# Kernel tuning notes

Measured on AMD Instinct MI355X. Metric: run time of the kernel, lower is better.

## Reference

```python
import jax, jax.numpy as jnp
import numpy as np

V = 8000; TZ = 128; TU = 256; B = 64; H = 1024; E = 512; DG = 64
GI = E + 2 * H + DG  # GRU input size = embed + z_ctx + u_ctx + degree


def _build_sparse_z(rng):
    # faithful vectorized version of get_sparse_selective_input (minus vocab SLOT branch)
    z_np = rng.integers(0, V + 10, size=(TZ, B))  # some ids >= V -> OOV copy path
    res = np.full((TZ, B, V + TZ), 1e-10, np.float32)
    w = z_np[:-1]                                   # [TZ-1, B]
    cond = (w == 2) | (w >= V)
    ti, bi = np.meshgrid(np.arange(TZ - 1), np.arange(B), indexing='ij')
    col = np.where(cond, V + ti, w)
    val = np.where(cond, np.float32(5.0), np.float32(1.0))
    res[ti + 1, bi, col] = val
    return jnp.asarray(res.transpose(1, 0, 2))      # [B, TZ, V+TZ]


def setup_inputs():
    key = jax.random.key(0)
    ks = jax.random.split(key, 16)
    s = 0.02
    iv = 1.0 / np.sqrt(H)
    return dict(
        z_enc_out=jax.random.normal(ks[0], (TZ, B, H), jnp.float32),
        u_enc_out=jax.random.normal(ks[1], (TU, B, H), jnp.float32),
        m_t_input=jax.random.randint(ks[2], (1, B), 0, V),
        degree_input=jax.random.normal(ks[3], (B, DG), jnp.float32),
        last_hidden=jax.random.normal(ks[4], (1, B, H), jnp.float32),
        sparse_z_input=_build_sparse_z(np.random.default_rng(0)),
        emb_W=jax.random.normal(ks[5], (V, E), jnp.float32) * s,
        attn_z_W=jax.random.normal(ks[6], (H, 2 * H), jnp.float32) * s,
        attn_z_b=jnp.zeros((H,), jnp.float32),
        attn_z_v=jax.random.normal(ks[7], (H,), jnp.float32) * iv,
        attn_u_W=jax.random.normal(ks[8], (H, 2 * H), jnp.float32) * s,
        attn_u_b=jnp.zeros((H,), jnp.float32),
        attn_u_v=jax.random.normal(ks[9], (H,), jnp.float32) * iv,
        gru_Wih=jax.random.normal(ks[10], (3 * H, GI), jnp.float32) * s,
        gru_Whh=jax.random.normal(ks[11], (3 * H, H), jnp.float32) * s,
        gru_bih=jnp.zeros((3 * H,), jnp.float32),
        gru_bhh=jnp.zeros((3 * H,), jnp.float32),
        proj_W=jax.random.normal(ks[12], (V, 3 * H), jnp.float32) * s,
        proj_b=jnp.zeros((V,), jnp.float32),
        copy2_W=jax.random.normal(ks[13], (H, H), jnp.float32) * s,
        copy2_b=jnp.zeros((H,), jnp.float32),
    )


def _attn(hidden, enc, W, b, v):
    # hidden [1,B,H], enc [T,B,H] -> context [1,B,H] (Bahdanau additive attention)
    enc_b = jnp.transpose(enc, (1, 0, 2))                       # [B,T,H]
    Hrep = jnp.broadcast_to(jnp.transpose(hidden, (1, 0, 2)), enc_b.shape)
    energy = jnp.tanh(jnp.concatenate([Hrep, enc_b], -1) @ W.T + b)  # [B,T,H]
    scores = jnp.einsum('bth,h->bt', energy, v)[:, None, :]    # [B,1,T]
    alpha = jax.nn.softmax(scores, axis=2)
    ctx = jnp.einsum('bit,bth->bih', alpha, enc_b)              # [B,1,H]
    return jnp.transpose(ctx, (1, 0, 2))                        # [1,B,H]


def _gru_step(x, h, Wih, Whh, bih, bhh):
    # single step, torch gate order (r, z, n)
    gi = x @ Wih.T + bih
    gh = h @ Whh.T + bhh
    ir, iz, inn = jnp.split(gi, 3, -1)
    hr, hz, hn = jnp.split(gh, 3, -1)
    r = jax.nn.sigmoid(ir + hr)
    z = jax.nn.sigmoid(iz + hz)
    n = jnp.tanh(inn + r * hn)
    return (1.0 - z) * n + z * h


def reference(z_enc_out, u_enc_out, m_t_input, degree_input, last_hidden,
              sparse_z_input, emb_W, attn_z_W, attn_z_b, attn_z_v,
              attn_u_W, attn_u_b, attn_u_v, gru_Wih, gru_Whh, gru_bih, gru_bhh,
              proj_W, proj_b, copy2_W, copy2_b):
    m_embed = emb_W[m_t_input]                                  # [1,B,E]
    z_ctx = _attn(last_hidden, z_enc_out, attn_z_W, attn_z_b, attn_z_v)  # [1,B,H]
    u_ctx = _attn(last_hidden, u_enc_out, attn_u_W, attn_u_b, attn_u_v)  # [1,B,H]
    gru_in = jnp.concatenate([m_embed, u_ctx, z_ctx, degree_input[None]], axis=2)
    gru_out = _gru_step(gru_in, last_hidden, gru_Wih, gru_Whh, gru_bih, gru_bhh)
    new_hidden = gru_out                                        # single-layer GRU, 1 step
    gen_score = (jnp.concatenate([z_ctx, u_ctx, gru_out], 2) @ proj_W.T + proj_b)[0]  # [B,V]
    # pointer copy scores over z encoder states
    z_cs = jnp.tanh(jnp.transpose(z_enc_out, (1, 0, 2)) @ copy2_W.T + copy2_b)  # [B,TZ,H]
    z_cs = jnp.einsum('bth,bh->bt', z_cs, gru_out[0])           # [B,TZ]
    m = jnp.max(z_cs, axis=1, keepdims=True)
    e = jnp.exp(z_cs - m)
    z_copy = jnp.log(jnp.einsum('bt,btv->bv', e, sparse_z_input)) + m  # [B,V+TZ]
    scores = jax.nn.softmax(jnp.concatenate([gen_score, z_copy], axis=1), axis=1)
    gen_s, zc = scores[:, :V], scores[:, V:]
    proba = jnp.concatenate([gen_s + zc[:, :V], zc[:, V:]], axis=1)  # [B, V+TZ]
    return (proba, new_hidden, gru_out)
```

## Files before the change

kernel.cpp:

```cpp
#include <hip/hip_runtime.h>
#include <cmath>

#define B64 64
#define H 1024
#define E 512
#define DG 64
#define GIN 2624
#define TZ 128
#define TU 256
#define V 8000
#define VT 8128
#define NC 16128

using bf16x8 = __attribute__((ext_vector_type(8))) short;
using f32x4  = __attribute__((ext_vector_type(4))) float;

__device__ inline unsigned pack2(float a, float b) {
    unsigned ua = __float_as_uint(a) + 0x8000u;
    unsigned ub = __float_as_uint(b) + 0x8000u;
    return __builtin_amdgcn_perm(ub, ua, 0x07060302u);
}
__device__ inline uint2 pack4(float4 v) {
    return make_uint2(pack2(v.x, v.y), pack2(v.z, v.w));
}

__device__ inline float fast_tanh(float x) {
    float e = __expf(2.f * x);
    return 1.f - 2.f / (e + 1.f);
}
__device__ inline float fast_sig(float x) {
    return 1.f / (1.f + __expf(-x));
}

__device__ inline void gl_lds16(const void* gptr, void* lptr) {
    __builtin_amdgcn_global_load_lds(
        (const __attribute__((address_space(1))) void*)gptr,
        (__attribute__((address_space(3))) void*)lptr, 16, 0, 0);
}

__device__ __forceinline__ void gemm_core(
    short (*As)[40], short (*Bs)[40], int tid,
    const float* __restrict__ A, int lda,
    const float* __restrict__ W, int ldw, int koff,
    const float* __restrict__ bias,
    float* __restrict__ C, int N,
    int n0, int kb, int ke, bool addbias)
{
    const int wave = tid >> 6, lane = tid & 63;
    const int wm = wave >> 1, wn = wave & 1;
    const int q = lane >> 4, l16 = lane & 15;

    f32x4 acc[2][2];
#pragma unroll
    for (int i = 0; i < 2; ++i)
#pragma unroll
        for (int j = 0; j < 2; ++j) acc[i][j] = f32x4{0.f, 0.f, 0.f, 0.f};

    for (int ks = kb; ks < ke; ++ks) {
        const int k0 = ks * 32;
        __syncthreads();
#pragma unroll
        for (int i = 0; i < 2; ++i) {
            int slot = i * 256 + tid;
            int row  = slot >> 3;
            int kq   = (slot & 7) << 2;
            float4 a = *(const float4*)(A + (size_t)row * lda + k0 + kq);
            *(uint2*)&As[row][kq] = pack4(a);
            float4 w = *(const float4*)(W + (size_t)(n0 + row) * ldw + koff + k0 + kq);
            *(uint2*)&Bs[row][kq] = pack4(w);
        }
        __syncthreads();
        bf16x8 af[2], bfr[2];
#pragma unroll
        for (int t = 0; t < 2; ++t) af[t]  = *(bf16x8*)&As[wm * 32 + t * 16 + l16][q * 8];
#pragma unroll
        for (int t = 0; t < 2; ++t) bfr[t] = *(bf16x8*)&Bs[wn * 32 + t * 16 + l16][q * 8];
#pragma unroll
        for (int tm = 0; tm < 2; ++tm)
#pragma unroll
            for (int tn = 0; tn < 2; ++tn)
                acc[tm][tn] = __builtin_amdgcn_mfma_f32_16x16x32_bf16(
                    af[tm], bfr[tn], acc[tm][tn], 0, 0, 0);
    }

#pragma unroll
    for (int tm = 0; tm < 2; ++tm) {
#pragma unroll
        for (int r = 0; r < 4; ++r) {
            int b = wm * 32 + tm * 16 + q * 4 + r;
#pragma unroll
            for (int tn = 0; tn < 2; ++tn) {
                int n = n0 + wn * 32 + tn * 16 + l16;
                float v = acc[tm][tn][r];
                if (addbias) v += bias[n];
                atomicAdd(&C[(size_t)b * N + n], v);
            }
        }
    }
}

__global__ __launch_bounds__(256) void k_prep(
    const float* __restrict__ u_enc, const float* __restrict__ z_enc,
    const float* __restrict__ azW, const float* __restrict__ auW,
    const float* __restrict__ c2W,
    unsigned short* __restrict__ ubf, unsigned short* __restrict__ zbf,
    unsigned short* __restrict__ azWbf, unsigned short* __restrict__ auWbf,
    unsigned short* __restrict__ c2Wbf,
    const int* __restrict__ mt, const float* __restrict__ embW,
    const float* __restrict__ degree, float* __restrict__ x,
    const float* __restrict__ h0,
    const float* __restrict__ azb, float* __restrict__ hbz,
    const float* __restrict__ aub, float* __restrict__ hbu,
    const float* __restrict__ Whh, const float* __restrict__ bhh,
    float* __restrict__ gh)
{
    __shared__ short As[64][40];
    __shared__ short Bs[64][40];
    int n = blockIdx.x, tid = threadIdx.x;
    if (n < 640) {
        const float *W, *bias; float* C; int ldw, N, n0, kc;
        if (n < 128)      { W = azW; bias = azb; C = hbz; ldw = 2048; N = 1024; n0 = (n & 15) * 64;  kc = n >> 4; }
        else if (n < 256) { int m = n - 128; W = auW; bias = aub; C = hbu; ldw = 2048; N = 1024; n0 = (m & 15) * 64; kc = m >> 4; }
        else              { int m = n - 256; W = Whh; bias = bhh; C = gh;  ldw = 1024; N = 3072; n0 = (m % 48) * 64; kc = m / 48; }
        gemm_core(As, Bs, tid, h0, 1024, W, ldw, 0, bias, C, N, n0, kc * 4, kc * 4 + 4, kc == 0);
        return;
    }
    n -= 640;
    if (n >= 27648) {
        int b = n - 27648;
        int m = mt[b];
        for (int k = tid; k < E; k += 256) x[(size_t)b * GIN + k] = embW[(size_t)m * E + k];
        if (tid < DG) x[(size_t)b * GIN + E + 2 * H + tid] = degree[b * DG + tid];
        return;
    }
    int k4 = tid * 4;
    const float* src; unsigned short* dst; int ld, koff, r;
    if (n < 16384)      { src = u_enc; dst = ubf;   ld = 1024; koff = 0;    r = n; }
    else if (n < 24576) { src = z_enc; dst = zbf;   ld = 1024; koff = 0;    r = n - 16384; }
    else if (n < 25600) { src = azW;   dst = azWbf; ld = 2048; koff = 1024; r = n - 24576; }
    else if (n < 26624) { src = auW;   dst = auWbf; ld = 2048; koff = 1024; r = n - 25600; }
    else                { src = c2W;   dst = c2Wbf; ld = 1024; koff = 0;    r = n - 26624; }
    float4 v = *(const float4*)(src + (size_t)r * ld + koff + k4);
    *(uint2*)(dst + (size_t)r * 1024 + k4) = pack4(v);
}

__global__ __launch_bounds__(256) void ftd_all(
    const unsigned short* __restrict__ zbf_, const unsigned short* __restrict__ ubf_,
    const unsigned short* __restrict__ azWbf, const unsigned short* __restrict__ auWbf,
    const unsigned short* __restrict__ c2Wbf,
    const float* __restrict__ hbz, const float* __restrict__ hbu,
    const float* __restrict__ azv, const float* __restrict__ auv,
    const float* __restrict__ c2b,
    float* __restrict__ scores_z, float* __restrict__ scores_u,
    float* __restrict__ tz)
{
    __shared__ unsigned short As[128 * 32];
    __shared__ unsigned short Bs[128 * 32];
    const int tid  = threadIdx.x;
    const int wave = tid >> 6, lane = tid & 63;
    const int wm = wave >> 1, wn = wave & 1;
    const int q = lane >> 4, l16 = lane & 15;
    const int lrow = lane >> 2;
    const int lk   = (lane & 3) * 8;

    const int gid = blockIdx.x;
    const bool isU = gid >= 1024;
    int m0, n0;
    const unsigned short *A, *W;
    bool isTZ = false;
    const float* addv; const float* vvec; float* outs;
    if (isU) {
        int g = gid - 1024;
        m0 = (g & 127) * 128;
        n0 = (g >> 7) * 128;
        A = ubf_; W = auWbf;
        addv = hbu; vvec = auv; outs = scores_u;
    } else {
        m0 = (gid & 63) * 128;
        int by = gid >> 6;
        A = zbf_;
        if (by < 8) { n0 = by * 128; W = azWbf; addv = hbz; vvec = azv; outs = scores_z; }
        else        { n0 = (by - 8) * 128; W = c2Wbf; isTZ = true; addv = nullptr; vvec = nullptr; outs = nullptr; }
    }

    f32x4 acc[4][4];
#pragma unroll
    for (int i = 0; i < 4; ++i)
#pragma unroll
        for (int j = 0; j < 4; ++j) acc[i][j] = f32x4{0.f, 0.f, 0.f, 0.f};

    for (int kt = 0; kt < 32; ++kt) {
        const int k0 = kt * 32;
        __syncthreads();
#pragma unroll
        for (int j = 0; j < 2; ++j) {
            int r0 = (wave * 2 + j) * 16;
            gl_lds16(A + (size_t)(m0 + r0 + lrow) * 1024 + k0 + lk, &As[r0 * 32]);
            gl_lds16(W + (size_t)(n0 + r0 + lrow) * 1024 + k0 + lk, &Bs[r0 * 32]);
        }
        __syncthreads();
        bf16x8 af[4], bfr[4];
#pragma unroll
        for (int t = 0; t < 4; ++t) af[t]  = *(bf16x8*)&As[(wm * 64 + t * 16 + l16) * 32 + q * 8];
#pragma unroll
        for (int t = 0; t < 4; ++t) bfr[t] = *(bf16x8*)&Bs[(wn * 64 + t * 16 + l16) * 32 + q * 8];
#pragma unroll
        for (int tm = 0; tm < 4; ++tm)
#pragma unroll
            for (int tn = 0; tn < 4; ++tn)
                acc[tm][tn] = __builtin_amdgcn_mfma_f32_16x16x32_bf16(
                    af[tm], bfr[tn], acc[tm][tn], 0, 0, 0);
    }

    if (!isTZ) {
#pragma unroll
        for (int tm = 0; tm < 4; ++tm) {
#pragma unroll
            for (int r = 0; r < 4; ++r) {
                int R = m0 + wm * 64 + tm * 16 + q * 4 + r;
                int b = R & 63;
                float s = 0.f;
#pragma unroll
                for (int tn = 0; tn < 4; ++tn) {
                    int col = n0 + wn * 64 + tn * 16 + l16;
                    float e = acc[tm][tn][r] + addv[(size_t)b * 1024 + col];
                    s += fast_tanh(e) * vvec[col];
                }
                s += __shfl_xor(s, 1);
                s += __shfl_xor(s, 2);
                s += __shfl_xor(s, 4);
                s += __shfl_xor(s, 8);
                if (l16 == 0) atomicAdd(&outs[R], s);
            }
        }
    } else {
#pragma unroll
        for (int tm = 0; tm < 4; ++tm) {
#pragma unroll
            for (int r = 0; r < 4; ++r) {
                int R = m0 + wm * 64 + tm * 16 + q * 4 + r;
#pragma unroll
                for (int tn = 0; tn < 4; ++tn) {
                    int col = n0 + wn * 64 + tn * 16 + l16;
                    tz[(size_t)R * 1024 + col] = fast_tanh(acc[tm][tn][r] + c2b[col]);
                }
            }
        }
    }
}

__global__ __launch_bounds__(256) void gemm_bt_mfma(
    const float* __restrict__ A, int lda,
    const float* __restrict__ W, int ldw, int koff,
    const float* __restrict__ bias,
    float* __restrict__ C, int N,
    int ks_total, int ks_chunk)
{
    __shared__ short As[64][40];
    __shared__ short Bs[64][40];
    int n0 = blockIdx.x * 64;
    int kb = blockIdx.y * ks_chunk;
    int ke = min(kb + ks_chunk, ks_total);
    gemm_core(As, Bs, threadIdx.x, A, lda, W, ldw, koff, bias, C, N,
              n0, kb, ke, blockIdx.y == 0);
}

__global__ __launch_bounds__(256) void k_softmax_ctx_bf(
    const float* __restrict__ scores_z, const float* __restrict__ scores_u,
    const unsigned short* __restrict__ zbf_, const unsigned short* __restrict__ ubf_,
    float* __restrict__ x, float* __restrict__ y)
{
    __shared__ float red[256];
    __shared__ float al[256];
    int b = blockIdx.x, tid = threadIdx.x;
    int side = blockIdx.y >> 1, hc = blockIdx.y & 1;
    const float* scores = side ? scores_u : scores_z;
    const unsigned short* encbf = side ? ubf_ : zbf_;
    int T = side ? TU : TZ;
    int xoff = side ? 512 : 1536;
    int yoff = side ? 1024 : 0;

    float s = (tid < T) ? scores[tid * B64 + b] : -1e30f;
    red[tid] = s; __syncthreads();
    for (int off = 128; off > 0; off >>= 1) {
        if (tid < off) red[tid] = fmaxf(red[tid], red[tid + off]);
        __syncthreads();
    }
    float mx = red[0]; __syncthreads();
    float e = (tid < T) ? __expf(s - mx) : 0.f;
    red[tid] = e; __syncthreads();
    for (int off = 128; off > 0; off >>= 1) {
        if (tid < off) red[tid] += red[tid + off];
        __syncthreads();
    }
    float inv = 1.f / red[0];
    al[tid] = e * inv;
    __syncthreads();
    int h = hc * 512 + tid * 2;
    float a0 = 0.f, a1 = 0.f;
#pragma unroll 4
    for (int t = 0; t < T; ++t) {
        unsigned u = *(const unsigned*)(encbf + ((size_t)t * B64 + b) * 1024 + h);
        float w = al[t];
        a0 += w * __uint_as_float(u << 16);
        a1 += w * __uint_as_float(u & 0xffff0000u);
    }
    x[(size_t)b * GIN + xoff + h]     = a0;
    x[(size_t)b * GIN + xoff + h + 1] = a1;
    y[(size_t)b * 3072 + yoff + h]     = a0;
    y[(size_t)b * 3072 + yoff + h + 1] = a1;
}

__global__ __launch_bounds__(512) void k_zcs_gate(
    const float* __restrict__ gi, const float* __restrict__ gh,
    const float* __restrict__ h0, const float* __restrict__ tz,
    float* __restrict__ zraw,
    float* __restrict__ y, float* __restrict__ out_hid,
    float* __restrict__ out_gru)
{
    __shared__ float g[1024];
    int b = blockIdx.x, quarter = blockIdx.y, tid = threadIdx.x;
    int wave = tid >> 6, lane = tid & 63;
    for (int j = tid; j < H; j += 512) {
        float ir = gi[(size_t)b * 3072 + j];
        float iz = gi[(size_t)b * 3072 + H + j];
        float in_ = gi[(size_t)b * 3072 + 2 * H + j];
        float hr = gh[(size_t)b * 3072 + j];
        float hz = gh[(size_t)b * 3072 + H + j];
        float hn = gh[(size_t)b * 3072 + 2 * H + j];
        float r = fast_sig(ir + hr);
        float z = fast_sig(iz + hz);
        float nn = fast_tanh(in_ + r * hn);
        float h = h0[(size_t)b * H + j];
        float o = (1.f - z) * nn + z * h;
        g[j] = o;
        if (quarter == 0) {
            y[(size_t)b * 3072 + 2 * H + j] = o;
            out_hid[(size_t)b * H + j] = o;
            out_gru[(size_t)b * H + j] = o;
        }
    }
    __syncthreads();
    float gr[16];
#pragma unroll
    for (int j = 0; j < 16; ++j) gr[j] = g[lane * 16 + j];
    int t0 = quarter * 32;
#pragma unroll
    for (int i = 0; i < 4; ++i) {
        int t = t0 + wave + i * 8;
        const float* row = tz + ((size_t)t * B64 + b) * 1024 + lane * 16;
        float s = 0.f;
#pragma unroll
        for (int c = 0; c < 4; ++c) {
            float4 v = *(const float4*)(row + c * 4);
            s += v.x * gr[c * 4 + 0] + v.y * gr[c * 4 + 1]
               + v.z * gr[c * 4 + 2] + v.w * gr[c * 4 + 3];
        }
#pragma unroll
        for (int off = 32; off > 0; off >>= 1) s += __shfl_xor(s, off);
        if (lane == 0) zraw[b * TZ + t] = s;
    }
}

__global__ __launch_bounds__(256) void k_gen_sparse(
    const float* __restrict__ y, const float* __restrict__ pW,
    const float* __restrict__ pb, float* __restrict__ gen,
    const float* __restrict__ sz, const float* __restrict__ zraw,
    float* __restrict__ zcopy)
{
    __shared__ short As[64][40];
    __shared__ short Bs[64][40];
    __shared__ float es[TZ];
    __shared__ float mred[2];
    int n = blockIdx.x, tid = threadIdx.x;
    if (n >= 512) {
        int gblk = n - 512;
        int n0 = (gblk % 125) * 64;
        int kc = gblk / 125;
        gemm_core(As, Bs, tid, y, 3072, pW, 3072, 0, pb, gen, 8000,
                  n0, kc * 12, kc * 12 + 12, kc == 0);
        return;
    }
    int c = n & 7, b = n >> 3;
    float sv = 0.f;
    if (tid < TZ) {
        sv = zraw[b * TZ + tid];
        float mm = sv;
#pragma unroll
        for (int off = 32; off > 0; off >>= 1) mm = fmaxf(mm, __shfl_xor(mm, off));
        if ((tid & 63) == 0) mred[tid >> 6] = mm;
    }
    __syncthreads();
    float m = fmaxf(mred[0], mred[1]);
    if (tid < TZ) es[tid] = __expf(sv - m);
    __syncthreads();
    if (tid >= 254) return;
    int v4 = c * 254 + tid;
    const f32x4* base = (const f32x4*)(sz + (size_t)b * TZ * VT);
    float4 acc = make_float4(0.f, 0.f, 0.f, 0.f);
#pragma unroll 16
    for (int t = 0; t < TZ; ++t) {
        f32x4 xv = __builtin_nontemporal_load(&base[(size_t)t * (VT / 4) + v4]);
        float e = es[t];
        acc.x += e * xv[0]; acc.y += e * xv[1]; acc.z += e * xv[2]; acc.w += e * xv[3];
    }
    int v = v4 * 4;
    zcopy[(size_t)b * VT + v + 0] = __logf(acc.x) + m;
    zcopy[(size_t)b * VT + v + 1] = __logf(acc.y) + m;
    zcopy[(size_t)b * VT + v + 2] = __logf(acc.z) + m;
    zcopy[(size_t)b * VT + v + 3] = __logf(acc.w) + m;
}

__global__ __launch_bounds__(1024) void k_final(
    const float* __restrict__ gen, const float* __restrict__ zcopy,
    float* __restrict__ proba)
{
    __shared__ float lg[NC];
    __shared__ float wred[16];
    int b = blockIdx.x, tid = threadIdx.x;
    int lane = tid & 63, wave = tid >> 6;
    for (int i = tid; i < V; i += 1024) lg[i] = gen[(size_t)b * V + i];
    for (int i = tid; i < VT; i += 1024) lg[V + i] = zcopy[(size_t)b * VT + i];
    __syncthreads();
    float mx = -1e30f;
    for (int i = tid; i < NC; i += 1024) mx = fmaxf(mx, lg[i]);
#pragma unroll
    for (int off = 32; off > 0; off >>= 1) mx = fmaxf(mx, __shfl_xor(mx, off));
    if (lane == 0) wred[wave] = mx;
    __syncthreads();
    mx = wred[0];
#pragma unroll
    for (int w = 1; w < 16; ++w) mx = fmaxf(mx, wred[w]);
    __syncthreads();
    float sm = 0.f;
    for (int i = tid; i < NC; i += 1024) sm += __expf(lg[i] - mx);
#pragma unroll
    for (int off = 32; off > 0; off >>= 1) sm += __shfl_xor(sm, off);
    if (lane == 0) wred[wave] = sm;
    __syncthreads();
    float Z = 0.f;
#pragma unroll
    for (int w = 0; w < 16; ++w) Z += wred[w];
    float invZ = 1.f / Z;
    for (int v = tid; v < VT; v += 1024) {
        float p = __expf(lg[V + v] - mx) * invZ;
        if (v < V) p += __expf(lg[v] - mx) * invZ;
        proba[(size_t)b * VT + v] = p;
    }
}

extern "C" void kernel_launch(void* const* d_in, const int* in_sizes, int n_in,
                              void* d_out, int out_size, void* d_ws, size_t ws_size,
                              hipStream_t stream)
{
    const float* z_enc  = (const float*)d_in[0];
    const float* u_enc  = (const float*)d_in[1];
    const int*   mt     = (const int*)d_in[2];
    const float* degree = (const float*)d_in[3];
    const float* h0     = (const float*)d_in[4];
    const float* sz     = (const float*)d_in[5];
    const float* embW   = (const float*)d_in[6];
    const float* azW    = (const float*)d_in[7];
    const float* azb    = (const float*)d_in[8];
    const float* azv    = (const float*)d_in[9];
    const float* auW    = (const float*)d_in[10];
    const float* aub    = (const float*)d_in[11];
    const float* auv    = (const float*)d_in[12];
    const float* Wih    = (const float*)d_in[13];
    const float* Whh    = (const float*)d_in[14];
    const float* bih    = (const float*)d_in[15];
    const float* bhh    = (const float*)d_in[16];
    const float* pW     = (const float*)d_in[17];
    const float* pb     = (const float*)d_in[18];
    const float* c2W    = (const float*)d_in[19];
    const float* c2b    = (const float*)d_in[20];

    float* ws       = (float*)d_ws;
    float* scores_z = ws;
    float* scores_u = ws + 8192;
    float* hbz      = ws + 32768;
    float* hbu      = ws + 98304;
    float* gi       = ws + 163840;
    float* gh       = ws + 360448;
    float* gen      = ws + 557056;
    float* x        = ws + 1069056;
    float* y        = ws + 1236992;
    float* zcopy    = ws + 1507392;
    float* tz       = ws + 2027584;
    unsigned short* ubf   = (unsigned short*)(ws + 2027584 + 8388608);
    unsigned short* zbf   = ubf + (size_t)16384 * 1024;
    unsigned short* azWbf = zbf + (size_t)8192 * 1024;
    unsigned short* auWbf = azWbf + (size_t)1024 * 1024;
    unsigned short* c2Wbf = auWbf + (size_t)1024 * 1024;
    float* zraw = ws + 24571968;

    float* out_proba = (float*)d_out;
    float* out_hid   = out_proba + (size_t)B64 * VT;
    float* out_gru   = out_hid + (size_t)B64 * H;

    hipMemsetAsync(ws, 0, 1069056 * sizeof(float), stream);

    k_prep<<<28352, 256, 0, stream>>>(u_enc, z_enc, azW, auW, c2W,
                                      ubf, zbf, azWbf, auWbf, c2Wbf,
                                      mt, embW, degree, x,
                                      h0, azb, hbz, aub, hbu, Whh, bhh, gh);

    ftd_all<<<2048, 256, 0, stream>>>(zbf, ubf, azWbf, auWbf, c2Wbf,
                                      hbz, hbu, azv, auv, c2b,
                                      scores_z, scores_u, tz);

    k_softmax_ctx_bf<<<dim3(64, 4), 256, 0, stream>>>(scores_z, scores_u, zbf, ubf, x, y);

    gemm_bt_mfma<<<dim3(48, 8), 256, 0, stream>>>(x, GIN, Wih, GIN, 0, bih, gi, 3072, 82, 11);

    k_zcs_gate<<<dim3(64, 4), 512, 0, stream>>>(gi, gh, h0, tz, zraw, y, out_hid, out_gru);

    k_gen_sparse<<<1512, 256, 0, stream>>>(y, pW, pb, gen, sz, zraw, zcopy);

    k_final<<<64, 1024, 0, stream>>>(gen, zcopy, out_proba);
}
```

Measured before the change: 744.4 us.

## Move ctx part of projection GEMM earlier, fuse memset into prep, store h0 GEMMs

The projection GEMM over the z_ctx/u_ctx columns (first 2048 K) now runs together with the GRU input GEMM in a new combined kernel, because it only needs y from the context kernel. The later gen kernel handles just the gru_out columns, which shortens the work left after the gate step. The h0 GEMMs in prep now cover all of K in each block and write results directly instead of using split-K atomics. The hipMemsetAsync is replaced by zeroing blocks inside k_prep. Risks: the h0 GEMMs now run on far fewer blocks (80), and correctness depends on the memset-replacement offsets covering every buffer that is later accumulated with atomics.

```diff
diff --git a/kernel.cpp b/kernel.cpp
--- a/kernel.cpp
+++ b/kernel.cpp
@@ -44,7 +44,7 @@
     const float* __restrict__ W, int ldw, int koff,
     const float* __restrict__ bias,
     float* __restrict__ C, int N,
-    int n0, int kb, int ke, bool addbias)
+    int n0, int kb, int ke, bool addbias, bool store)
 {
     const int wave = tid >> 6, lane = tid & 63;
     const int wm = wave >> 1, wn = wave & 1;
@@ -93,7 +93,8 @@
                 int n = n0 + wn * 32 + tn * 16 + l16;
                 float v = acc[tm][tn][r];
                 if (addbias) v += bias[n];
-                atomicAdd(&C[(size_t)b * N + n], v);
+                if (store) C[(size_t)b * N + n] = v;
+                else       atomicAdd(&C[(size_t)b * N + n], v);
             }
         }
     }
@@ -112,20 +113,29 @@
     const float* __restrict__ azb, float* __restrict__ hbz,
     const float* __restrict__ aub, float* __restrict__ hbu,
     const float* __restrict__ Whh, const float* __restrict__ bhh,
-    float* __restrict__ gh)
+    float* __restrict__ gh, float* __restrict__ ws)
 {
     __shared__ short As[64][40];
     __shared__ short Bs[64][40];
     int n = blockIdx.x, tid = threadIdx.x;
-    if (n < 640) {
-        const float *W, *bias; float* C; int ldw, N, n0, kc;
-        if (n < 128)      { W = azW; bias = azb; C = hbz; ldw = 2048; N = 1024; n0 = (n & 15) * 64;  kc = n >> 4; }
-        else if (n < 256) { int m = n - 128; W = auW; bias = aub; C = hbu; ldw = 2048; N = 1024; n0 = (m & 15) * 64; kc = m >> 4; }
-        else              { int m = n - 256; W = Whh; bias = bhh; C = gh;  ldw = 1024; N = 3072; n0 = (m % 48) * 64; kc = m / 48; }
-        gemm_core(As, Bs, tid, h0, 1024, W, ldw, 0, bias, C, N, n0, kc * 4, kc * 4 + 4, kc == 0);
+    if (n < 80) {
+        const float *W, *bias; float* C; int ldw, N, n0;
+        if (n < 16)      { W = azW; bias = azb; C = hbz; ldw = 2048; N = 1024; n0 = n * 64; }
+        else if (n < 32) { W = auW; bias = aub; C = hbu; ldw = 2048; N = 1024; n0 = (n - 16) * 64; }
+        else             { W = Whh; bias = bhh; C = gh;  ldw = 1024; N = 3072; n0 = (n - 32) * 64; }
+        gemm_core(As, Bs, tid, h0, 1024, W, ldw, 0, bias, C, N, n0, 0, 32, true, true);
         return;
     }
-    n -= 640;
+    if (n < 804) {
+        int zi = n - 80;
+        size_t off;
+        if (zi < 32)       off = (size_t)zi * 1024;
+        else if (zi < 224) off = 163840 + (size_t)(zi - 32) * 1024;
+        else               off = 557056 + (size_t)(zi - 224) * 1024;
+        *(f32x4*)(ws + off + tid * 4) = f32x4{0.f, 0.f, 0.f, 0.f};
+        return;
+    }
+    n -= 804;
     if (n >= 27648) {
         int b = n - 27648;
         int m = mt[b];
@@ -249,22 +259,6 @@
     }
 }
 
-__global__ __launch_bounds__(256) void gemm_bt_mfma(
-    const float* __restrict__ A, int lda,
-    const float* __restrict__ W, int ldw, int koff,
-    const float* __restrict__ bias,
-    float* __restrict__ C, int N,
-    int ks_total, int ks_chunk)
-{
-    __shared__ short As[64][40];
-    __shared__ short Bs[64][40];
-    int n0 = blockIdx.x * 64;
-    int kb = blockIdx.y * ks_chunk;
-    int ke = min(kb + ks_chunk, ks_total);
-    gemm_core(As, Bs, threadIdx.x, A, lda, W, ldw, koff, bias, C, N,
-              n0, kb, ke, blockIdx.y == 0);
-}
-
 __global__ __launch_bounds__(256) void k_softmax_ctx_bf(
     const float* __restrict__ scores_z, const float* __restrict__ scores_u,
     const unsigned short* __restrict__ zbf_, const unsigned short* __restrict__ ubf_,
@@ -309,6 +303,30 @@
     x[(size_t)b * GIN + xoff + h + 1] = a1;
     y[(size_t)b * 3072 + yoff + h]     = a0;
     y[(size_t)b * 3072 + yoff + h + 1] = a1;
+}
+
+__global__ __launch_bounds__(256) void k_gi_genA(
+    const float* __restrict__ x, const float* __restrict__ Wih,
+    const float* __restrict__ bih, float* __restrict__ gi,
+    const float* __restrict__ y, const float* __restrict__ pW,
+    float* __restrict__ gen)
+{
+    __shared__ short As[64][40];
+    __shared__ short Bs[64][40];
+    int n = blockIdx.x, tid = threadIdx.x;
+    if (n < 500) {
+        int n0 = (n % 125) * 64;
+        int kc = n / 125;
+        gemm_core(As, Bs, tid, y, 3072, pW, 3072, 0, nullptr, gen, 8000,
+                  n0, kc * 16, kc * 16 + 16, false, false);
+    } else {
+        int g = n - 500;
+        int n0 = (g % 48) * 64;
+        int kc = g / 48;
+        int kb = kc * 11, ke = min(kb + 11, 82);
+        gemm_core(As, Bs, tid, x, GIN, Wih, GIN, 0, bih, gi, 3072,
+                  n0, kb, ke, kc == 0, false);
+    }
 }
 
 __global__ __launch_bounds__(512) void k_zcs_gate(
@@ -374,11 +392,12 @@
     __shared__ float mred[2];
     int n = blockIdx.x, tid = threadIdx.x;
     if (n >= 512) {
-        int gblk = n - 512;
-        int n0 = (gblk % 125) * 64;
-        int kc = gblk / 125;
+        int g = n - 512;
+        int n0 = (g % 125) * 64;
+        int kc = g / 125;
+        int kb = 64 + kc * 16;
         gemm_core(As, Bs, tid, y, 3072, pW, 3072, 0, pb, gen, 8000,
-                  n0, kc * 12, kc * 12 + 12, kc == 0);
+                  n0, kb, kb + 16, kc == 0, false);
         return;
     }
     int c = n & 7, b = n >> 3;
@@ -498,12 +517,10 @@
     float* out_hid   = out_proba + (size_t)B64 * VT;
     float* out_gru   = out_hid + (size_t)B64 * H;
 
-    hipMemsetAsync(ws, 0, 1069056 * sizeof(float), stream);
-
-    k_prep<<<28352, 256, 0, stream>>>(u_enc, z_enc, azW, auW, c2W,
+    k_prep<<<28516, 256, 0, stream>>>(u_enc, z_enc, azW, auW, c2W,
                                       ubf, zbf, azWbf, auWbf, c2Wbf,
                                       mt, embW, degree, x,
-                                      h0, azb, hbz, aub, hbu, Whh, bhh, gh);
+                                      h0, azb, hbz, aub, hbu, Whh, bhh, gh, ws);
 
     ftd_all<<<2048, 256, 0, stream>>>(zbf, ubf, azWbf, auWbf, c2Wbf,
                                       hbz, hbu, azv, auv, c2b,
@@ -511,11 +528,11 @@
 
     k_softmax_ctx_bf<<<dim3(64, 4), 256, 0, stream>>>(scores_z, scores_u, zbf, ubf, x, y);
 
-    gemm_bt_mfma<<<dim3(48, 8), 256, 0, stream>>>(x, GIN, Wih, GIN, 0, bih, gi, 3072, 82, 11);
+    k_gi_genA<<<884, 256, 0, stream>>>(x, Wih, bih, gi, y, pW, gen);
 
     k_zcs_gate<<<dim3(64, 4), 512, 0, stream>>>(gi, gh, h0, tz, zraw, y, out_hid, out_gru);
 
-    k_gen_sparse<<<1512, 256, 0, stream>>>(y, pW, pb, gen, sz, zraw, zcopy);
+    k_gen_sparse<<<762, 256, 0, stream>>>(y, pW, pb, gen, sz, zraw, zcopy);
 
     k_final<<<64, 1024, 0, stream>>>(gen, zcopy, out_proba);
 }
```

Measured after the change: 792.5 us. 1.06x slower.
